# Optimization experiments

Hardware: AMD Instinct MI355X
Metric: run time of the kernel (lower is better)

The kernel has to match this reference:

```python
import jax, jax.numpy as jnp
import numpy as np
from jax import lax

K = 3          # kernel size
PAD = 1        # 'same' padding for k=3: (1,1,1,1)
STRIDE = 1
DIL = 1
OFFSET_SIZE = 2 * K * K  # deformable_groups=1


def setup_inputs() -> dict:
    key = jax.random.key(0)
    k1, k2, k3, k4 = jax.random.split(key, 4)
    B, H, W, C = 8, 64, 64, 256
    F = 256
    inputs = jax.random.normal(k1, (B, H, W, C), dtype=jnp.float32)
    # offset/mask branch conv: small weights so sampled offsets are modest
    om_kernel = jax.random.normal(k2, (K, K, C, OFFSET_SIZE * 3 // 2), dtype=jnp.float32) * 0.01
    om_bias = jnp.zeros((OFFSET_SIZE * 3 // 2,), dtype=jnp.float32)
    stdv = 1.0 / np.sqrt(K * K * C)
    kernel = jax.random.uniform(k3, (K * K * C, F), dtype=jnp.float32, minval=-stdv, maxval=stdv)
    bias = jax.random.normal(k4, (1, 1, 1, F), dtype=jnp.float32) * 0.01
    return {"inputs": inputs, "om_kernel": om_kernel, "om_bias": om_bias,
            "kernel": kernel, "bias": bias}


def _dcnv2(x, om_kernel, om_bias, kernel, bias):
    B, H, W, C = x.shape
    # offset/mask branch (same conv geometry as the deformable conv)
    om = lax.conv_general_dilated(
        x, om_kernel, window_strides=(STRIDE, STRIDE),
        padding=((PAD, PAD), (PAD, PAD)), rhs_dilation=(DIL, DIL),
        dimension_numbers=('NHWC', 'HWIO', 'NHWC')) + om_bias
    OH, OW = om.shape[1], om.shape[2]
    KK = K * K
    offset = om[..., :OFFSET_SIZE].reshape(B, OH, OW, KK, 2)  # (dy, dx) per kernel point
    mask = jax.nn.sigmoid(om[..., OFFSET_SIZE:]) * 2.0         # [B,OH,OW,KK]

    # base sampling grid per output pixel and kernel point
    kk = jnp.arange(KK)
    ky = (kk // K).astype(jnp.float32)
    kx = (kk % K).astype(jnp.float32)
    base_y = jnp.arange(OH, dtype=jnp.float32)[:, None] * STRIDE - PAD + ky[None, :] * DIL  # [OH,KK]
    base_x = jnp.arange(OW, dtype=jnp.float32)[:, None] * STRIDE - PAD + kx[None, :] * DIL  # [OW,KK]

    py = base_y[None, :, None, :] + offset[..., 0]  # [B,OH,OW,KK]
    px = base_x[None, None, :, :] + offset[..., 1]

    y0 = jnp.floor(py); x0 = jnp.floor(px)
    wy1 = py - y0; wy0 = 1.0 - wy1
    wx1 = px - x0; wx0 = 1.0 - wx1

    bi = jnp.arange(B)[:, None, None, None]

    def gather(yi, xi):
        # zero-padded bilinear corner fetch
        valid = (yi >= 0) & (yi <= H - 1) & (xi >= 0) & (xi <= W - 1)
        yc = jnp.clip(yi, 0, H - 1).astype(jnp.int32)
        xc = jnp.clip(xi, 0, W - 1).astype(jnp.int32)
        v = x[bi, yc, xc]  # [B,OH,OW,KK,C]
        return v * valid[..., None].astype(x.dtype)

    y1 = y0 + 1.0; x1 = x0 + 1.0
    cols = (gather(y0, x0) * (wy0 * wx0)[..., None]
            + gather(y0, x1) * (wy0 * wx1)[..., None]
            + gather(y1, x0) * (wy1 * wx0)[..., None]
            + gather(y1, x1) * (wy1 * wx1)[..., None])
    cols = cols * mask[..., None]  # modulation, [B,OH,OW,KK,C]

    out = cols.reshape(B, OH, OW, KK * C) @ kernel  # [B,OH,OW,F]
    return out + bias


def reference(inputs, om_kernel, om_bias, kernel, bias):
    return _dcnv2(inputs, om_kernel, om_bias, kernel, bias)
```

## Files before the change

### kernel.cpp

```cpp
#include <hip/hip_runtime.h>
#include <math.h>


#define BB 8
#define HH 64
#define WW 64
#define CIN 256
#define FF 256
#define KPTS 9
#define OCH 27
#define MT 32
#define NS2 36

typedef _Float16 half8  __attribute__((ext_vector_type(8)));
typedef _Float16 half4v __attribute__((ext_vector_type(4)));
typedef float    floatx4 __attribute__((ext_vector_type(4)));

__device__ __forceinline__ int aoff(int m, int g) {
    return m * 64 + ((g ^ (m & 7)) << 3);
}

__device__ __forceinline__ half8 splat8(_Float16 v) {
    half8 r = {v, v, v, v, v, v, v, v};
    return r;
}

#define XBLK 4096
__global__ __launch_bounds__(256) void convert_all(
    const float* __restrict__ x, const float* __restrict__ wmat,
    const float* __restrict__ omw,
    _Float16* __restrict__ xh, _Float16* __restrict__ wsB, _Float16* __restrict__ wsOM)
{
    const int bid = blockIdx.x;
    if (bid < XBLK) {
        if (xh == nullptr) return;
        const size_t i = ((size_t)bid * 256 + threadIdx.x) * 8;
        const floatx4 a = *(const floatx4*)(x + i);
        const floatx4 b = *(const floatx4*)(x + i + 4);
        half8 h;
        h[0] = (_Float16)a.x; h[1] = (_Float16)a.y; h[2] = (_Float16)a.z; h[3] = (_Float16)a.w;
        h[4] = (_Float16)b.x; h[5] = (_Float16)b.y; h[6] = (_Float16)b.z; h[7] = (_Float16)b.w;
        *(half8*)(xh + i) = h;
    } else if (bid < XBLK + 288) {
        const int kg = bid - XBLK;
        const int n  = threadIdx.x;
        half8 h;
        #pragma unroll
        for (int j = 0; j < 8; ++j)
            h[j] = (_Float16)wmat[(size_t)(kg * 8 + j) * FF + n];
        ((half8*)wsB)[(size_t)kg * FF + n] = h;
    } else {
        const int t = (bid - XBLK - 288) * 256 + threadIdx.x;
        const int k = t >> 5, n = t & 31;
        const float v = (n < OCH) ? omw[k * OCH + n] : 0.f;
        wsOM[((size_t)(k >> 3) * 32 + n) * 8 + (k & 7)] = (_Float16)v;
    }
}

template <bool F16X>
__global__ __launch_bounds__(256, 4) void dcn_mfma5(
    const float* __restrict__ x,
    const _Float16* __restrict__ xh,
    const float* __restrict__ omb,
    const _Float16* __restrict__ wsB,
    const _Float16* __restrict__ wsOM,
    const float* __restrict__ bias,
    float* __restrict__ out)
{
    __shared__ _Float16 Ah0[MT * 64];
    __shared__ _Float16 Ah1[MT * 64];
    __shared__ float    om_s[MT][28];
    __shared__ half4v   cwS[MT][KPTS];
    __shared__ int4     caS[MT][KPTS];

    const int tid  = threadIdx.x;
    const int w    = tid >> 6;
    const int lane = tid & 63;
    const int q    = lane >> 4;
    const int lr   = lane & 15;
    const int ms   = tid >> 3;
    const int qc   = tid & 7;

    const int p   = blockIdx.x;
    const int b   = p & 7;
    const int r   = p >> 3;
    const int oh  = r >> 1;
    const int owb = (r & 1) * MT;
    const int pbase = (b * HH + oh) * WW + owb;

    const half8* wsOM8 = (const half8*)wsOM;
    const half8* wsB8  = (const half8*)wsB;

    const int mt1 = w & 1;
    const int nt1 = w >> 1;
    floatx4 acc1 = {0.f, 0.f, 0.f, 0.f};

    auto load1 = [&](int sp) -> half8 {
        sp = sp < NS2 - 1 ? sp : NS2 - 1;
        const int kk = sp >> 2, cb = (sp & 3) << 6;
        const int ky = kk / 3, kx = kk - ky * 3;
        const int iy = oh - 1 + ky, ix = owb + ms - 1 + kx;
        half8 v = {(_Float16)0, (_Float16)0, (_Float16)0, (_Float16)0,
                   (_Float16)0, (_Float16)0, (_Float16)0, (_Float16)0};
        if (iy >= 0 && iy < HH && ix >= 0 && ix < WW) {
            const int idx = ((b * HH + iy) * WW + ix) * CIN + cb + qc * 8;
            if constexpr (F16X) {
                v = *(const half8*)(xh + idx);
            } else {
                const floatx4 lo = *(const floatx4*)(x + idx);
                const floatx4 hi = *(const floatx4*)(x + idx + 4);
                v[0] = (_Float16)lo.x; v[1] = (_Float16)lo.y;
                v[2] = (_Float16)lo.z; v[3] = (_Float16)lo.w;
                v[4] = (_Float16)hi.x; v[5] = (_Float16)hi.y;
                v[6] = (_Float16)hi.z; v[7] = (_Float16)hi.w;
            }
        }
        return v;
    };
    auto loadB1 = [&](int sp, half8& b0, half8& b1) {
        sp = sp < NS2 - 1 ? sp : NS2 - 1;
        b0 = wsOM8[(sp * 8 + q) * 32 + nt1 * 16 + lr];
        b1 = wsOM8[(sp * 8 + 4 + q) * 32 + nt1 * 16 + lr];
    };

    half8 vp;
    half8 bo00, bo01, bo10, bo11;
    {
        const half8 v0 = load1(0);
        *(half8*)(Ah0 + aoff(ms, qc)) = v0;
        vp = load1(1);
        loadB1(0, bo00, bo01);
    }
    for (int s = 0; s < NS2; s += 2) {
        __syncthreads();
        *(half8*)(Ah1 + aoff(ms, qc)) = vp;
        vp = load1(s + 2);
        loadB1(s + 1, bo10, bo11);
        {
            const half8 a0 = *(const half8*)(Ah0 + aoff(mt1 * 16 + lr, q));
            const half8 a1 = *(const half8*)(Ah0 + aoff(mt1 * 16 + lr, 4 + q));
            acc1 = __builtin_amdgcn_mfma_f32_16x16x32_f16(a0, bo00, acc1, 0, 0, 0);
            acc1 = __builtin_amdgcn_mfma_f32_16x16x32_f16(a1, bo01, acc1, 0, 0, 0);
        }
        __syncthreads();
        *(half8*)(Ah0 + aoff(ms, qc)) = vp;
        vp = load1(s + 3);
        loadB1(s + 2, bo00, bo01);
        {
            const half8 a0 = *(const half8*)(Ah1 + aoff(mt1 * 16 + lr, q));
            const half8 a1 = *(const half8*)(Ah1 + aoff(mt1 * 16 + lr, 4 + q));
            acc1 = __builtin_amdgcn_mfma_f32_16x16x32_f16(a0, bo10, acc1, 0, 0, 0);
            acc1 = __builtin_amdgcn_mfma_f32_16x16x32_f16(a1, bo11, acc1, 0, 0, 0);
        }
    }
    {
        const int och = nt1 * 16 + lr;
        if (och < OCH) {
            const float ob = omb[och];
            #pragma unroll
            for (int reg = 0; reg < 4; ++reg) {
                const int m = mt1 * 16 + q * 4 + reg;
                om_s[m][och] = acc1[reg] + ob;
            }
        }
    }
    __syncthreads();

    for (int i = tid; i < MT * KPTS; i += 256) {
        const int m = i / KPTS, kk = i % KPTS;
        const int ky = kk / 3, kx = kk - ky * 3;
        const float dy = om_s[m][2 * kk];
        const float dx = om_s[m][2 * kk + 1];
        const float mask = 2.f / (1.f + __expf(-om_s[m][18 + kk]));
        const float py = (float)(oh - 1 + ky) + dy;
        const float px = (float)(owb + m - 1 + kx) + dx;
        const float y0f = floorf(py), x0f = floorf(px);
        const float wy1 = py - y0f, wx1 = px - x0f;
        const float wy0 = 1.f - wy1, wx0 = 1.f - wx1;
        const int y0 = (int)y0f, x0 = (int)x0f;
        const int y1 = y0 + 1, x1 = x0 + 1;
        const bool vy0 = (y0 >= 0) && (y0 < HH);
        const bool vy1 = (y1 >= 0) && (y1 < HH);
        const bool vx0 = (x0 >= 0) && (x0 < WW);
        const bool vx1 = (x1 >= 0) && (x1 < WW);
        const int y0c = min(max(y0, 0), HH - 1), y1c = min(max(y1, 0), HH - 1);
        const int x0c = min(max(x0, 0), WW - 1), x1c = min(max(x1, 0), WW - 1);
        const int rb = b * HH;
        int4 ca;
        ca.x = ((rb + y0c) * WW + x0c) * CIN;
        ca.y = ((rb + y0c) * WW + x1c) * CIN;
        ca.z = ((rb + y1c) * WW + x0c) * CIN;
        ca.w = ((rb + y1c) * WW + x1c) * CIN;
        half4v cw;
        cw.x = (_Float16)((vy0 && vx0) ? mask * wy0 * wx0 : 0.f);
        cw.y = (_Float16)((vy0 && vx1) ? mask * wy0 * wx1 : 0.f);
        cw.z = (_Float16)((vy1 && vx0) ? mask * wy1 * wx0 : 0.f);
        cw.w = (_Float16)((vy1 && vx1) ? mask * wy1 * wx1 : 0.f);
        caS[m][kk] = ca;
        cwS[m][kk] = cw;
    }
    __syncthreads();

    floatx4 acc[2][4];
    #pragma unroll
    for (int t = 0; t < 2; ++t)
        #pragma unroll
        for (int nt = 0; nt < 4; ++nt)
            acc[t][nt] = (floatx4){0.f, 0.f, 0.f, 0.f};

    const int n0w = w * 64;

    half8   pc0, pc1, pc2, pc3;
    floatx4 fa0, fb0, fa1, fb1, fa2, fb2, fa3, fb3;
    half4v  pcw;

    auto pre2 = [&](int sp) {
        sp = sp < NS2 - 1 ? sp : NS2 - 1;
        const int kk = sp >> 2;
        const int co = ((sp & 3) << 6) + qc * 8;
        const int4 ca = caS[ms][kk];
        pcw = cwS[ms][kk];
        if constexpr (F16X) {
            pc0 = *(const half8*)(xh + ca.x + co);
            pc1 = *(const half8*)(xh + ca.y + co);
            pc2 = *(const half8*)(xh + ca.z + co);
            pc3 = *(const half8*)(xh + ca.w + co);
        } else {
            fa0 = *(const floatx4*)(x + ca.x + co); fb0 = *(const floatx4*)(x + ca.x + co + 4);
            fa1 = *(const floatx4*)(x + ca.y + co); fb1 = *(const floatx4*)(x + ca.y + co + 4);
            fa2 = *(const floatx4*)(x + ca.z + co); fb2 = *(const floatx4*)(x + ca.z + co + 4);
            fa3 = *(const floatx4*)(x + ca.w + co); fb3 = *(const floatx4*)(x + ca.w + co + 4);
        }
    };
    auto comb = [&]() -> half8 {
        if constexpr (F16X) {
            const half8 w0 = splat8(pcw.x), w1 = splat8(pcw.y);
            const half8 w2 = splat8(pcw.z), w3 = splat8(pcw.w);
            return pc0 * w0 + pc1 * w1 + pc2 * w2 + pc3 * w3;
        } else {
            const float w0 = (float)pcw.x, w1 = (float)pcw.y;
            const float w2 = (float)pcw.z, w3 = (float)pcw.w;
            const floatx4 lo = w0 * fa0 + w1 * fa1 + w2 * fa2 + w3 * fa3;
            const floatx4 hi = w0 * fb0 + w1 * fb1 + w2 * fb2 + w3 * fb3;
            half8 r;
            r[0] = (_Float16)lo.x; r[1] = (_Float16)lo.y;
            r[2] = (_Float16)lo.z; r[3] = (_Float16)lo.w;
            r[4] = (_Float16)hi.x; r[5] = (_Float16)hi.y;
            r[6] = (_Float16)hi.z; r[7] = (_Float16)hi.w;
            return r;
        }
    };

    half8 bP[2][4];
    auto loadB2 = [&](int sp) {
        const int kk = sp >> 2;
        const int r8 = kk * 32 + (sp & 3) * 8;
        #pragma unroll
        for (int kh = 0; kh < 2; ++kh)
            #pragma unroll
            for (int nt = 0; nt < 4; ++nt)
                bP[kh][nt] = wsB8[(size_t)(r8 + kh * 4 + q) * FF + n0w + nt * 16 + lr];
    };

    {
        pre2(0);
        const half8 v0 = comb();
        *(half8*)(Ah0 + aoff(ms, qc)) = v0;
        pre2(1);
    }
    for (int s = 0; s < NS2; s += 2) {
        __syncthreads();
        {
            const half8 v = comb();
            *(half8*)(Ah1 + aoff(ms, qc)) = v;
        }
        loadB2(s);
        pre2(s + 2);
        #pragma unroll
        for (int kh = 0; kh < 2; ++kh) {
            half8 afr[2];
            #pragma unroll
            for (int t = 0; t < 2; ++t)
                afr[t] = *(const half8*)(Ah0 + aoff(t * 16 + lr, kh * 4 + q));
            #pragma unroll
            for (int nt = 0; nt < 4; ++nt)
                #pragma unroll
                for (int t = 0; t < 2; ++t)
                    acc[t][nt] = __builtin_amdgcn_mfma_f32_16x16x32_f16(afr[t], bP[kh][nt], acc[t][nt], 0, 0, 0);
        }
        __syncthreads();
        {
            const half8 v = comb();
            *(half8*)(Ah0 + aoff(ms, qc)) = v;
        }
        loadB2(s + 1);
        pre2(s + 3);
        #pragma unroll
        for (int kh = 0; kh < 2; ++kh) {
            half8 afr[2];
            #pragma unroll
            for (int t = 0; t < 2; ++t)
                afr[t] = *(const half8*)(Ah1 + aoff(t * 16 + lr, kh * 4 + q));
            #pragma unroll
            for (int nt = 0; nt < 4; ++nt)
                #pragma unroll
                for (int t = 0; t < 2; ++t)
                    acc[t][nt] = __builtin_amdgcn_mfma_f32_16x16x32_f16(afr[t], bP[kh][nt], acc[t][nt], 0, 0, 0);
        }
    }

    #pragma unroll
    for (int nt = 0; nt < 4; ++nt) {
        const int f = n0w + nt * 16 + lr;
        const float bv = bias[f];
        #pragma unroll
        for (int t = 0; t < 2; ++t)
            #pragma unroll
            for (int reg = 0; reg < 4; ++reg) {
                const int m = t * 16 + q * 4 + reg;
                out[(size_t)(pbase + m) * FF + f] = acc[t][nt][reg] + bv;
            }
    }
}

#define MTILE 32
#define CHUNK 64
#define NCHUNK (CIN / CHUNK)

__global__ __launch_bounds__(256) void dcn_fused(
    const float* __restrict__ x, const float* __restrict__ omw,
    const float* __restrict__ omb, const float* __restrict__ wmat,
    const float* __restrict__ bias, float* __restrict__ out)
{
    __shared__ float A[CHUNK][MTILE + 1];
    __shared__ float om_s[MTILE][28];
    __shared__ float cw[MTILE][4];
    __shared__ int   ca[MTILE][4];

    const int tid = threadIdx.x;
    const int pbase = blockIdx.x * MTILE;
    const int ccid = tid & 63;
    const int mg2 = tid >> 6;
    const int och = tid & 31;
    const int mg1 = tid >> 5;
    float acc1[4] = {0.f, 0.f, 0.f, 0.f};

    for (int kk = 0; kk < KPTS; ++kk) {
        const int ky = kk / 3, kx = kk % 3;
        for (int ch = 0; ch < NCHUNK; ++ch) {
            const int cbase = ch * CHUNK;
            __syncthreads();
            #pragma unroll
            for (int i = 0; i < 8; ++i) {
                const int m = mg2 * 8 + i;
                const int pp = pbase + m;
                const int bb = pp >> 12, oh = (pp >> 6) & 63, ow = pp & 63;
                const int iy = oh - 1 + ky, ix = ow - 1 + kx;
                float v = 0.f;
                if (iy >= 0 && iy < HH && ix >= 0 && ix < WW)
                    v = x[((bb * HH + iy) * WW + ix) * CIN + cbase + ccid];
                A[ccid][m] = v;
            }
            __syncthreads();
            if (och < OCH) {
                for (int cc = 0; cc < CHUNK; ++cc) {
                    const float bv = omw[((kk * CIN) + cbase + cc) * OCH + och];
                    #pragma unroll
                    for (int i = 0; i < 4; ++i)
                        acc1[i] += A[cc][mg1 * 4 + i] * bv;
                }
            }
        }
    }
    __syncthreads();
    if (och < OCH) {
        const float ob = omb[och];
        #pragma unroll
        for (int i = 0; i < 4; ++i)
            om_s[mg1 * 4 + i][och] = acc1[i] + ob;
    }
    __syncthreads();

    const int f4 = (tid & 63) * 4;
    const int mgc = tid >> 6;
    float acc[8][4];
    #pragma unroll
    for (int j = 0; j < 8; ++j)
        #pragma unroll
        for (int i = 0; i < 4; ++i) acc[j][i] = 0.f;

    for (int kk = 0; kk < KPTS; ++kk) {
        if (tid < MTILE) {
            const int m = tid;
            const int pp = pbase + m;
            const int bb = pp >> 12, oh = (pp >> 6) & 63, ow = pp & 63;
            const int ky = kk / 3, kx = kk % 3;
            const float dy = om_s[m][2 * kk];
            const float dx = om_s[m][2 * kk + 1];
            const float mask = 2.f / (1.f + __expf(-om_s[m][18 + kk]));
            const float py = (float)(oh - 1 + ky) + dy;
            const float px = (float)(ow - 1 + kx) + dx;
            const float y0f = floorf(py), x0f = floorf(px);
            const float wy1 = py - y0f, wx1 = px - x0f;
            const float wy0 = 1.f - wy1, wx0 = 1.f - wx1;
            const int y0 = (int)y0f, x0 = (int)x0f;
            const int y1 = y0 + 1, x1 = x0 + 1;
            const bool vy0 = (y0 >= 0) && (y0 < HH);
            const bool vy1 = (y1 >= 0) && (y1 < HH);
            const bool vx0 = (x0 >= 0) && (x0 < WW);
            const bool vx1 = (x1 >= 0) && (x1 < WW);
            const int y0c = min(max(y0, 0), HH - 1), y1c = min(max(y1, 0), HH - 1);
            const int x0c = min(max(x0, 0), WW - 1), x1c = min(max(x1, 0), WW - 1);
            const int rb = bb * HH;
            ca[m][0] = ((rb + y0c) * WW + x0c) * CIN;
            ca[m][1] = ((rb + y0c) * WW + x1c) * CIN;
            ca[m][2] = ((rb + y1c) * WW + x0c) * CIN;
            ca[m][3] = ((rb + y1c) * WW + x1c) * CIN;
            cw[m][0] = (vy0 && vx0) ? mask * wy0 * wx0 : 0.f;
            cw[m][1] = (vy0 && vx1) ? mask * wy0 * wx1 : 0.f;
            cw[m][2] = (vy1 && vx0) ? mask * wy1 * wx0 : 0.f;
            cw[m][3] = (vy1 && vx1) ? mask * wy1 * wx1 : 0.f;
        }
        for (int ch = 0; ch < NCHUNK; ++ch) {
            const int cbase = ch * CHUNK;
            __syncthreads();
            #pragma unroll
            for (int i = 0; i < 8; ++i) {
                const int m = mg2 * 8 + i;
                const int cidx = cbase + ccid;
                const float v = cw[m][0] * x[ca[m][0] + cidx]
                              + cw[m][1] * x[ca[m][1] + cidx]
                              + cw[m][2] * x[ca[m][2] + cidx]
                              + cw[m][3] * x[ca[m][3] + cidx];
                A[ccid][m] = v;
            }
            __syncthreads();
            const float* brow = wmat + (size_t)(kk * CIN + cbase) * FF + f4;
            for (int cc = 0; cc < CHUNK; ++cc) {
                const float4 bv = *(const float4*)(brow + cc * FF);
                #pragma unroll
                for (int j = 0; j < 8; ++j) {
                    const float a = A[cc][mgc * 8 + j];
                    acc[j][0] += a * bv.x;
                    acc[j][1] += a * bv.y;
                    acc[j][2] += a * bv.z;
                    acc[j][3] += a * bv.w;
                }
            }
        }
    }

    const float4 bb4 = *(const float4*)(bias + f4);
    #pragma unroll
    for (int j = 0; j < 8; ++j) {
        const int m = mgc * 8 + j;
        const int pp = pbase + m;
        float4 o;
        o.x = acc[j][0] + bb4.x;
        o.y = acc[j][1] + bb4.y;
        o.z = acc[j][2] + bb4.z;
        o.w = acc[j][3] + bb4.w;
        *(float4*)(out + (size_t)pp * FF + f4) = o;
    }
}

extern "C" void kernel_launch(void* const* d_in, const int* in_sizes, int n_in,
                              void* d_out, int out_size, void* d_ws, size_t ws_size,
                              hipStream_t stream) {
    const float* x    = (const float*)d_in[0];
    const float* omw  = (const float*)d_in[1];
    const float* omb  = (const float*)d_in[2];
    const float* wmat = (const float*)d_in[3];
    const float* bias = (const float*)d_in[4];
    float* out = (float*)d_out;

    const size_t needB  = (size_t)2304 * FF * sizeof(_Float16);
    const size_t needOM = (size_t)288 * 32 * 8 * sizeof(_Float16);
    const size_t needX  = (size_t)BB * HH * WW * CIN * sizeof(_Float16);

    if (ws_size >= needB + needOM + needX) {
        _Float16* wsB  = (_Float16*)d_ws;
        _Float16* wsOM = (_Float16*)((char*)d_ws + needB);
        _Float16* xh   = (_Float16*)((char*)d_ws + needB + needOM);
        convert_all<<<XBLK + 288 + 288, 256, 0, stream>>>(x, wmat, omw, xh, wsB, wsOM);
        dcn_mfma5<true><<<BB * HH * 2, 256, 0, stream>>>(x, xh, omb, wsB, wsOM, bias, out);
    } else if (ws_size >= needB + needOM) {
        _Float16* wsB  = (_Float16*)d_ws;
        _Float16* wsOM = (_Float16*)((char*)d_ws + needB);
        convert_all<<<XBLK + 288 + 288, 256, 0, stream>>>(x, wmat, omw, nullptr, wsB, wsOM);
        dcn_mfma5<false><<<BB * HH * 2, 256, 0, stream>>>(x, nullptr, omb, wsB, wsOM, bias, out);
    } else {
        const int nblocks = (BB * HH * WW) / MTILE;
        dcn_fused<<<nblocks, 256, 0, stream>>>(x, omw, omb, wmat, bias, out);
    }
}
```

Baseline: 163.4 us.

## Fuse fp16 conversion and DCN compute into one cooperative kernel with grid sync

Merges the conversion pre-pass (x, weight and offset-weight to fp16) into the main kernel, launched cooperatively with a grid-wide barrier before the compute body, so one launch replaces two. The gather/B-operand pipelines are also reworked into explicit even/odd double-buffered registers that prefetch two stages ahead. This removes a kernel launch boundary and the tail of the conversion pass, but needs all 1024 blocks co-resident for the cooperative launch, adds a grid barrier, and raises register pressure. If the cooperative launch fails, it falls back to the two-kernel path. The fp32-fallback path without an fp16 workspace is dropped.

After: 291.4 us. +78.3%, slower.

```diff
diff --git a/kernel.cpp b/kernel.cpp
--- a/kernel.cpp
+++ b/kernel.cpp
@@ -1,5 +1,8 @@
 #include <hip/hip_runtime.h>
+#include <hip/hip_cooperative_groups.h>
 #include <math.h>
+
+namespace cg = cooperative_groups;
 
 
 #define BB 8
@@ -25,41 +28,9 @@
     return r;
 }
 
-#define XBLK 4096
-__global__ __launch_bounds__(256) void convert_all(
-    const float* __restrict__ x, const float* __restrict__ wmat,
-    const float* __restrict__ omw,
-    _Float16* __restrict__ xh, _Float16* __restrict__ wsB, _Float16* __restrict__ wsOM)
-{
-    const int bid = blockIdx.x;
-    if (bid < XBLK) {
-        if (xh == nullptr) return;
-        const size_t i = ((size_t)bid * 256 + threadIdx.x) * 8;
-        const floatx4 a = *(const floatx4*)(x + i);
-        const floatx4 b = *(const floatx4*)(x + i + 4);
-        half8 h;
-        h[0] = (_Float16)a.x; h[1] = (_Float16)a.y; h[2] = (_Float16)a.z; h[3] = (_Float16)a.w;
-        h[4] = (_Float16)b.x; h[5] = (_Float16)b.y; h[6] = (_Float16)b.z; h[7] = (_Float16)b.w;
-        *(half8*)(xh + i) = h;
-    } else if (bid < XBLK + 288) {
-        const int kg = bid - XBLK;
-        const int n  = threadIdx.x;
-        half8 h;
-        #pragma unroll
-        for (int j = 0; j < 8; ++j)
-            h[j] = (_Float16)wmat[(size_t)(kg * 8 + j) * FF + n];
-        ((half8*)wsB)[(size_t)kg * FF + n] = h;
-    } else {
-        const int t = (bid - XBLK - 288) * 256 + threadIdx.x;
-        const int k = t >> 5, n = t & 31;
-        const float v = (n < OCH) ? omw[k * OCH + n] : 0.f;
-        wsOM[((size_t)(k >> 3) * 32 + n) * 8 + (k & 7)] = (_Float16)v;
-    }
-}
-
-template <bool F16X>
-__global__ __launch_bounds__(256, 4) void dcn_mfma5(
-    const float* __restrict__ x,
+#define ZERO8 {(_Float16)0,(_Float16)0,(_Float16)0,(_Float16)0,(_Float16)0,(_Float16)0,(_Float16)0,(_Float16)0}
+
+__device__ __forceinline__ void dcn_body(
     const _Float16* __restrict__ xh,
     const float* __restrict__ omb,
     const _Float16* __restrict__ wsB,
@@ -100,21 +71,9 @@
         const int kk = sp >> 2, cb = (sp & 3) << 6;
         const int ky = kk / 3, kx = kk - ky * 3;
         const int iy = oh - 1 + ky, ix = owb + ms - 1 + kx;
-        half8 v = {(_Float16)0, (_Float16)0, (_Float16)0, (_Float16)0,
-                   (_Float16)0, (_Float16)0, (_Float16)0, (_Float16)0};
-        if (iy >= 0 && iy < HH && ix >= 0 && ix < WW) {
-            const int idx = ((b * HH + iy) * WW + ix) * CIN + cb + qc * 8;
-            if constexpr (F16X) {
-                v = *(const half8*)(xh + idx);
-            } else {
-                const floatx4 lo = *(const floatx4*)(x + idx);
-                const floatx4 hi = *(const floatx4*)(x + idx + 4);
-                v[0] = (_Float16)lo.x; v[1] = (_Float16)lo.y;
-                v[2] = (_Float16)lo.z; v[3] = (_Float16)lo.w;
-                v[4] = (_Float16)hi.x; v[5] = (_Float16)hi.y;
-                v[6] = (_Float16)hi.z; v[7] = (_Float16)hi.w;
-            }
-        }
+        half8 v = ZERO8;
+        if (iy >= 0 && iy < HH && ix >= 0 && ix < WW)
+            v = *(const half8*)(xh + ((b * HH + iy) * WW + ix) * CIN + cb + qc * 8);
         return v;
     };
     auto loadB1 = [&](int sp, half8& b0, half8& b1) {
@@ -123,35 +82,35 @@
         b1 = wsOM8[(sp * 8 + 4 + q) * 32 + nt1 * 16 + lr];
     };
 
-    half8 vp;
-    half8 bo00, bo01, bo10, bo11;
-    {
-        const half8 v0 = load1(0);
-        *(half8*)(Ah0 + aoff(ms, qc)) = v0;
-        vp = load1(1);
-        loadB1(0, bo00, bo01);
-    }
+    half8 vpE, vpO, boE0, boE1, boO0, boO1;
+    vpE = load1(0);
+    vpO = load1(1);
+    loadB1(0, boE0, boE1);
+    loadB1(1, boO0, boO1);
+    *(half8*)(Ah0 + aoff(ms, qc)) = vpE;
+    vpE = load1(2);
+
     for (int s = 0; s < NS2; s += 2) {
         __syncthreads();
-        *(half8*)(Ah1 + aoff(ms, qc)) = vp;
-        vp = load1(s + 2);
-        loadB1(s + 1, bo10, bo11);
+        *(half8*)(Ah1 + aoff(ms, qc)) = vpO;
+        vpO = load1(s + 3);
         {
             const half8 a0 = *(const half8*)(Ah0 + aoff(mt1 * 16 + lr, q));
             const half8 a1 = *(const half8*)(Ah0 + aoff(mt1 * 16 + lr, 4 + q));
-            acc1 = __builtin_amdgcn_mfma_f32_16x16x32_f16(a0, bo00, acc1, 0, 0, 0);
-            acc1 = __builtin_amdgcn_mfma_f32_16x16x32_f16(a1, bo01, acc1, 0, 0, 0);
-        }
+            acc1 = __builtin_amdgcn_mfma_f32_16x16x32_f16(a0, boE0, acc1, 0, 0, 0);
+            acc1 = __builtin_amdgcn_mfma_f32_16x16x32_f16(a1, boE1, acc1, 0, 0, 0);
+        }
+        loadB1(s + 2, boE0, boE1);
         __syncthreads();
-        *(half8*)(Ah0 + aoff(ms, qc)) = vp;
-        vp = load1(s + 3);
-        loadB1(s + 2, bo00, bo01);
+        *(half8*)(Ah0 + aoff(ms, qc)) = vpE;
+        vpE = load1(s + 4);
         {
             const half8 a0 = *(const half8*)(Ah1 + aoff(mt1 * 16 + lr, q));
             const half8 a1 = *(const half8*)(Ah1 + aoff(mt1 * 16 + lr, 4 + q));
-            acc1 = __builtin_amdgcn_mfma_f32_16x16x32_f16(a0, bo10, acc1, 0, 0, 0);
-            acc1 = __builtin_amdgcn_mfma_f32_16x16x32_f16(a1, bo11, acc1, 0, 0, 0);
-        }
+            acc1 = __builtin_amdgcn_mfma_f32_16x16x32_f16(a0, boO0, acc1, 0, 0, 0);
+            acc1 = __builtin_amdgcn_mfma_f32_16x16x32_f16(a1, boO1, acc1, 0, 0, 0);
+        }
+        loadB1(s + 3, boO0, boO1);
     }
     {
         const int och = nt1 * 16 + lr;
@@ -210,45 +169,30 @@
 
     const int n0w = w * 64;
 
-    half8   pc0, pc1, pc2, pc3;
-    floatx4 fa0, fb0, fa1, fb1, fa2, fb2, fa3, fb3;
-    half4v  pcw;
-
-    auto pre2 = [&](int sp) {
+    half8  pcE0, pcE1, pcE2, pcE3, pcO0, pcO1, pcO2, pcO3;
+    half4v pcwE, pcwO;
+
+    auto pre2E = [&](int sp) {
         sp = sp < NS2 - 1 ? sp : NS2 - 1;
         const int kk = sp >> 2;
         const int co = ((sp & 3) << 6) + qc * 8;
         const int4 ca = caS[ms][kk];
-        pcw = cwS[ms][kk];
-        if constexpr (F16X) {
-            pc0 = *(const half8*)(xh + ca.x + co);
-            pc1 = *(const half8*)(xh + ca.y + co);
-            pc2 = *(const half8*)(xh + ca.z + co);
-            pc3 = *(const half8*)(xh + ca.w + co);
-        } else {
-            fa0 = *(const floatx4*)(x + ca.x + co); fb0 = *(const floatx4*)(x + ca.x + co + 4);
-            fa1 = *(const floatx4*)(x + ca.y + co); fb1 = *(const floatx4*)(x + ca.y + co + 4);
-            fa2 = *(const floatx4*)(x + ca.z + co); fb2 = *(const floatx4*)(x + ca.z + co + 4);
-            fa3 = *(const floatx4*)(x + ca.w + co); fb3 = *(const floatx4*)(x + ca.w + co + 4);
-        }
+        pcwE = cwS[ms][kk];
+        pcE0 = *(const half8*)(xh + ca.x + co);
+        pcE1 = *(const half8*)(xh + ca.y + co);
+        pcE2 = *(const half8*)(xh + ca.z + co);
+        pcE3 = *(const half8*)(xh + ca.w + co);
     };
-    auto comb = [&]() -> half8 {
-        if constexpr (F16X) {
-            const half8 w0 = splat8(pcw.x), w1 = splat8(pcw.y);
-            const half8 w2 = splat8(pcw.z), w3 = splat8(pcw.w);
-            return pc0 * w0 + pc1 * w1 + pc2 * w2 + pc3 * w3;
-        } else {
-            const float w0 = (float)pcw.x, w1 = (float)pcw.y;
-            const float w2 = (float)pcw.z, w3 = (float)pcw.w;
-            const floatx4 lo = w0 * fa0 + w1 * fa1 + w2 * fa2 + w3 * fa3;
-            const floatx4 hi = w0 * fb0 + w1 * fb1 + w2 * fb2 + w3 * fb3;
-            half8 r;
-            r[0] = (_Float16)lo.x; r[1] = (_Float16)lo.y;
-            r[2] = (_Float16)lo.z; r[3] = (_Float16)lo.w;
-            r[4] = (_Float16)hi.x; r[5] = (_Float16)hi.y;
-            r[6] = (_Float16)hi.z; r[7] = (_Float16)hi.w;
-            return r;
-        }
+    auto pre2O = [&](int sp) {
+        sp = sp < NS2 - 1 ? sp : NS2 - 1;
+        const int kk = sp >> 2;
+        const int co = ((sp & 3) << 6) + qc * 8;
+        const int4 ca = caS[ms][kk];
+        pcwO = cwS[ms][kk];
+        pcO0 = *(const half8*)(xh + ca.x + co);
+        pcO1 = *(const half8*)(xh + ca.y + co);
+        pcO2 = *(const half8*)(xh + ca.z + co);
+        pcO3 = *(const half8*)(xh + ca.w + co);
     };
 
     half8 bP[2][4];
@@ -262,20 +206,24 @@
                 bP[kh][nt] = wsB8[(size_t)(r8 + kh * 4 + q) * FF + n0w + nt * 16 + lr];
     };
 
+    pre2E(0);
+    pre2O(1);
     {
-        pre2(0);
-        const half8 v0 = comb();
-        *(half8*)(Ah0 + aoff(ms, qc)) = v0;
-        pre2(1);
-    }
+        const half8 v = pcE0 * splat8(pcwE.x) + pcE1 * splat8(pcwE.y)
+                      + pcE2 * splat8(pcwE.z) + pcE3 * splat8(pcwE.w);
+        *(half8*)(Ah0 + aoff(ms, qc)) = v;
+    }
+    pre2E(2);
+
     for (int s = 0; s < NS2; s += 2) {
         __syncthreads();
         {
-            const half8 v = comb();
+            const half8 v = pcO0 * splat8(pcwO.x) + pcO1 * splat8(pcwO.y)
+                          + pcO2 * splat8(pcwO.z) + pcO3 * splat8(pcwO.w);
             *(half8*)(Ah1 + aoff(ms, qc)) = v;
         }
+        pre2O(s + 3);
         loadB2(s);
-        pre2(s + 2);
         #pragma unroll
         for (int kh = 0; kh < 2; ++kh) {
             half8 afr[2];
@@ -290,11 +238,12 @@
         }
         __syncthreads();
         {
-            const half8 v = comb();
+            const half8 v = pcE0 * splat8(pcwE.x) + pcE1 * splat8(pcwE.y)
+                          + pcE2 * splat8(pcwE.z) + pcE3 * splat8(pcwE.w);
             *(half8*)(Ah0 + aoff(ms, qc)) = v;
         }
+        pre2E(s + 4);
         loadB2(s + 1);
-        pre2(s + 3);
         #pragma unroll
         for (int kh = 0; kh < 2; ++kh) {
             half8 afr[2];
@@ -321,6 +270,80 @@
                 out[(size_t)(pbase + m) * FF + f] = acc[t][nt][reg] + bv;
             }
     }
+}
+
+__global__ __launch_bounds__(256, 4) void dcn_coop(
+    const float* __restrict__ x, const float* __restrict__ wmat,
+    const float* __restrict__ omw,
+    _Float16* __restrict__ xh, _Float16* __restrict__ wsB, _Float16* __restrict__ wsOM,
+    const float* __restrict__ omb, const float* __restrict__ bias,
+    float* __restrict__ out)
+{
+    const int p = blockIdx.x;
+    #pragma unroll
+    for (int j = 0; j < 4; ++j) {
+        const size_t i = (((size_t)p * 4 + j) * 256 + threadIdx.x) * 8;
+        const floatx4 a = *(const floatx4*)(x + i);
+        const floatx4 c = *(const floatx4*)(x + i + 4);
+        half8 h;
+        h[0] = (_Float16)a.x; h[1] = (_Float16)a.y; h[2] = (_Float16)a.z; h[3] = (_Float16)a.w;
+        h[4] = (_Float16)c.x; h[5] = (_Float16)c.y; h[6] = (_Float16)c.z; h[7] = (_Float16)c.w;
+        *(half8*)(xh + i) = h;
+    }
+    if (p < 288) {
+        const int kg = p, n = threadIdx.x;
+        half8 h;
+        #pragma unroll
+        for (int j = 0; j < 8; ++j)
+            h[j] = (_Float16)wmat[(size_t)(kg * 8 + j) * FF + n];
+        ((half8*)wsB)[(size_t)kg * FF + n] = h;
+    } else if (p < 576) {
+        const int t = (p - 288) * 256 + threadIdx.x;
+        const int k = t >> 5, n = t & 31;
+        const float v = (n < OCH) ? omw[k * OCH + n] : 0.f;
+        wsOM[((size_t)(k >> 3) * 32 + n) * 8 + (k & 7)] = (_Float16)v;
+    }
+    cg::this_grid().sync();
+    dcn_body(xh, omb, wsB, wsOM, bias, out);
+}
+
+#define XBLK 4096
+__global__ __launch_bounds__(256) void convert_all(
+    const float* __restrict__ x, const float* __restrict__ wmat,
+    const float* __restrict__ omw,
+    _Float16* __restrict__ xh, _Float16* __restrict__ wsB, _Float16* __restrict__ wsOM)
+{
+    const int bid = blockIdx.x;
+    if (bid < XBLK) {
+        const size_t i = ((size_t)bid * 256 + threadIdx.x) * 8;
+        const floatx4 a = *(const floatx4*)(x + i);
+        const floatx4 c = *(const floatx4*)(x + i + 4);
+        half8 h;
+        h[0] = (_Float16)a.x; h[1] = (_Float16)a.y; h[2] = (_Float16)a.z; h[3] = (_Float16)a.w;
+        h[4] = (_Float16)c.x; h[5] = (_Float16)c.y; h[6] = (_Float16)c.z; h[7] = (_Float16)c.w;
+        *(half8*)(xh + i) = h;
+    } else if (bid < XBLK + 288) {
+        const int kg = bid - XBLK;
+        const int n  = threadIdx.x;
+        half8 h;
+        #pragma unroll
+        for (int j = 0; j < 8; ++j)
+            h[j] = (_Float16)wmat[(size_t)(kg * 8 + j) * FF + n];
+        ((half8*)wsB)[(size_t)kg * FF + n] = h;
+    } else {
+        const int t = (bid - XBLK - 288) * 256 + threadIdx.x;
+        const int k = t >> 5, n = t & 31;
+        const float v = (n < OCH) ? omw[k * OCH + n] : 0.f;
+        wsOM[((size_t)(k >> 3) * 32 + n) * 8 + (k & 7)] = (_Float16)v;
+    }
+}
+
+__global__ __launch_bounds__(256, 4) void dcn_main(
+    const _Float16* __restrict__ xh, const float* __restrict__ omb,
+    const _Float16* __restrict__ wsB, const _Float16* __restrict__ wsOM,
+    const float* __restrict__ bias, float* __restrict__ out)
+{
+    dcn_body(xh, omb, wsB, wsOM, bias, out);
 }
 
 #define MTILE 32
@@ -482,13 +505,17 @@
         _Float16* wsB  = (_Float16*)d_ws;
         _Float16* wsOM = (_Float16*)((char*)d_ws + needB);
         _Float16* xh   = (_Float16*)((char*)d_ws + needB + needOM);
-        convert_all<<<XBLK + 288 + 288, 256, 0, stream>>>(x, wmat, omw, xh, wsB, wsOM);
-        dcn_mfma5<true><<<BB * HH * 2, 256, 0, stream>>>(x, xh, omb, wsB, wsOM, bias, out);
-    } else if (ws_size >= needB + needOM) {
-        _Float16* wsB  = (_Float16*)d_ws;
-        _Float16* wsOM = (_Float16*)((char*)d_ws + needB);
-        convert_all<<<XBLK + 288 + 288, 256, 0, stream>>>(x, wmat, omw, nullptr, wsB, wsOM);
-        dcn_mfma5<false><<<BB * HH * 2, 256, 0, stream>>>(x, nullptr, omb, wsB, wsOM, bias, out);
+
+        void* args[9] = { (void*)&x, (void*)&wmat, (void*)&omw,
+                          (void*)&xh, (void*)&wsB, (void*)&wsOM,
+                          (void*)&omb, (void*)&bias, (void*)&out };
+        hipError_t e = hipLaunchCooperativeKernel((const void*)dcn_coop,
+                                                  dim3(BB * HH * 2), dim3(256),
+                                                  args, 0, stream);
+        if (e != hipSuccess) {
+            convert_all<<<XBLK + 288 + 288, 256, 0, stream>>>(x, wmat, omw, xh, wsB, wsOM);
+            dcn_main<<<BB * HH * 2, 256, 0, stream>>>(xh, omb, wsB, wsOM, bias, out);
+        }
     } else {
         const int nblocks = (BB * HH * WW) / MTILE;
         dcn_fused<<<nblocks, 256, 0, stream>>>(x, omw, omb, wmat, bias, out);
```
